# Kernel tuning notes

Measured on AMD Instinct MI355X. Metric: run time of the kernel, lower is better.

## Reference

```python
import jax, jax.numpy as jnp
import numpy as np

B, S, E, H, L = 16, 1024, 512, 8, 4
D = E // H  # head_dim = 64


def setup_inputs() -> dict:
    key = jax.random.key(0)
    ks = jax.random.split(key, 16)
    std = 0.02
    inp = {
        "q": jax.random.normal(ks[0], (B, S, E), jnp.float32),
        "k": jax.random.normal(ks[1], (B, S, E), jnp.float32),
        "v": jax.random.normal(ks[2], (B, S, E), jnp.float32),
        # standard Linear params (torch convention: W is (out, in))
        "Wq": jax.random.normal(ks[3], (E, E), jnp.float32) * std,
        "bq": jnp.zeros((E,), jnp.float32),
        "Wk": jax.random.normal(ks[4], (E, E), jnp.float32) * std,
        "bk": jnp.zeros((E,), jnp.float32),
        # WFLinear: shared weight elementwise-multiplied by per-language factor
        "Wv_share": jax.random.normal(ks[5], (E, E), jnp.float32) * std,
        "Wv_spec": 1.0 + jax.random.normal(ks[6], (L, E, E), jnp.float32) * std,
        "bv_share": jnp.zeros((E,), jnp.float32),
        "bv_spec": jax.random.normal(ks[7], (L, E), jnp.float32) * std,
        "Wo_share": jax.random.normal(ks[8], (E, E), jnp.float32) * std,
        "Wo_spec": 1.0 + jax.random.normal(ks[9], (L, E, E), jnp.float32) * std,
        "bo_share": jnp.zeros((E,), jnp.float32),
        "bo_spec": jax.random.normal(ks[10], (L, E), jnp.float32) * std,
        "mask": jax.random.randint(ks[11], (B, S), 0, 2, jnp.int32),
        "languageID": 1,
    }
    return inp


def reference(q, k, v, Wq, bq, Wk, bk, Wv_share, Wv_spec, bv_share, bv_spec,
              Wo_share, Wo_spec, bo_share, bo_spec, mask, languageID):
    scaling = D ** (-0.5)
    # projections (torch Linear: x @ W.T + b)
    Q = (q @ Wq.T + bq).reshape(B, S, H, D).transpose(0, 2, 1, 3) * scaling
    K = (k @ Wk.T + bk).reshape(B, S, H, D).transpose(0, 2, 1, 3)
    Wv = Wv_share * Wv_spec[languageID]
    bv = bv_share + bv_spec[languageID]
    V = (v @ Wv.T + bv).reshape(B, S, H, D).transpose(0, 2, 1, 3)
    # NOTE: faithful to original — Q already scaled by d_k^-0.5, and
    # AttentionWF divides by sqrt(d_k) AGAIN (effective scale 1/d_k).
    alpha = jnp.einsum("bhqd,bhkd->bhqk", Q, K) / np.float32(np.sqrt(D))
    m = (mask == 0)[:, None, None, :]  # (B,1,1,S) over key axis
    alpha = jnp.where(m, jnp.float32(-1e9), alpha)
    alpha = jax.nn.softmax(alpha, axis=-1)
    # dropout p=0.0 -> identity
    ctx = jnp.einsum("bhqk,bhkd->bhqd", alpha, V)  # (B,H,S,D)
    concat = ctx.transpose(0, 2, 1, 3).reshape(B, S, E)
    Wo = Wo_share * Wo_spec[languageID]
    bo = bo_share + bo_spec[languageID]
    return concat @ Wo.T + bo
```

## Files before the change

### kernel.cpp

```cpp
#include <hip/hip_runtime.h>

#define B_ 16
#define S_ 1024
#define E_ 512
#define H_ 8
#define D_ 64
#define L_ 4
#define M_ (B_*S_)

typedef unsigned short u16;
typedef __attribute__((ext_vector_type(8))) short bf16x8;
typedef __attribute__((ext_vector_type(4))) float f32x4;

__device__ __forceinline__ u16 f2bf(float x) {
  unsigned u = __float_as_uint(x);
  unsigned r = (u + 0x7fffu + ((u >> 16) & 1u)) >> 16;
  return (u16)r;
}
__device__ __forceinline__ ushort4 f2bf4(float4 f) {
  ushort4 u;
  u.x = f2bf(f.x); u.y = f2bf(f.y); u.z = f2bf(f.z); u.w = f2bf(f.w);
  return u;
}

typedef __attribute__((address_space(1))) const void gconst_void;
typedef __attribute__((address_space(3))) void lds_void;
__device__ __forceinline__ void gl_lds16(const u16* g, u16* l) {
  __builtin_amdgcn_global_load_lds((gconst_void*)g, (lds_void*)l, 16, 0, 0);
}

__global__ __launch_bounds__(256) void cvt3(
    const float* __restrict__ a, const float* __restrict__ b, const float* __restrict__ c,
    u16* __restrict__ da, u16* __restrict__ db, u16* __restrict__ dc) {
  int i = blockIdx.x * 256 + threadIdx.x;
  const float* s = (blockIdx.y == 0) ? a : (blockIdx.y == 1) ? b : c;
  u16* d = (blockIdx.y == 0) ? da : (blockIdx.y == 1) ? db : dc;
  ((ushort4*)d)[i] = f2bf4(((const float4*)s)[i]);
}

__global__ __launch_bounds__(256) void prep_w(
    const float* __restrict__ Wq, const float* __restrict__ Wk,
    const float* __restrict__ Wv_sh, const float* __restrict__ Wv_sp,
    const float* __restrict__ Wo_sh, const float* __restrict__ Wo_sp,
    const float* __restrict__ bv_sh, const float* __restrict__ bv_sp,
    const float* __restrict__ bo_sh, const float* __restrict__ bo_sp,
    const int* __restrict__ langp,
    u16* __restrict__ Wq_b, u16* __restrict__ Wk_b,
    u16* __restrict__ Wv_b, u16* __restrict__ Wo_b,
    float* __restrict__ bv_f, float* __restrict__ bo_f) {
  int lang = langp[0];
  int i = blockIdx.x * 256 + threadIdx.x;
  size_t wofs = (size_t)lang * (E_*E_/4) + i;
  ((ushort4*)Wq_b)[i] = f2bf4(((const float4*)Wq)[i]);
  ((ushort4*)Wk_b)[i] = f2bf4(((const float4*)Wk)[i]);
  float4 vs = ((const float4*)Wv_sh)[i], vp = ((const float4*)Wv_sp)[wofs];
  float4 os = ((const float4*)Wo_sh)[i], op = ((const float4*)Wo_sp)[wofs];
  float4 vv = {vs.x*vp.x, vs.y*vp.y, vs.z*vp.z, vs.w*vp.w};
  float4 oo = {os.x*op.x, os.y*op.y, os.z*op.z, os.w*op.w};
  ((ushort4*)Wv_b)[i] = f2bf4(vv);
  ((ushort4*)Wo_b)[i] = f2bf4(oo);
  if (i < E_/4) {
    float4 b1 = ((const float4*)bv_sh)[i], b2 = ((const float4*)(bv_sp + (size_t)lang*E_))[i];
    float4 b3 = ((const float4*)bo_sh)[i], b4 = ((const float4*)(bo_sp + (size_t)lang*E_))[i];
    float4 r1 = {b1.x+b2.x, b1.y+b2.y, b1.z+b2.z, b1.w+b2.w};
    float4 r2 = {b3.x+b4.x, b3.y+b4.y, b3.z+b4.z, b3.w+b4.w};
    ((float4*)bv_f)[i] = r1;
    ((float4*)bo_f)[i] = r2;
  }
}

__global__ __launch_bounds__(256) void gemm_lds(
    const u16* __restrict__ A, const u16* __restrict__ Bw,
    const float* __restrict__ bias,
    void* __restrict__ out, int out_bf16, int Mdim, int Ndim, int Kdim) {
  __shared__ u16 sA[128*32];
  __shared__ u16 sB[128*32];
  const int t = threadIdx.x;
  const int m0 = blockIdx.y * 128, n0 = blockIdx.x * 128;
  const int lane = t & 63, wid = t >> 6;
  const int m16 = lane & 15, qq = lane >> 4;
  const int wrow = (wid >> 1) * 64, wcol = (wid & 1) * 64;
  f32x4 acc[4][4] = {};
  const int c0 = 2*wid, c1 = 2*wid + 1;
  const int colk = (lane & 3) * 8;
  const int r0 = c0*16 + (lane >> 2), r1 = c1*16 + (lane >> 2);
  const u16* a0 = A  + (size_t)(m0 + r0) * Kdim + colk;
  const u16* a1 = A  + (size_t)(m0 + r1) * Kdim + colk;
  const u16* b0 = Bw + (size_t)(n0 + r0) * Kdim + colk;
  const u16* b1 = Bw + (size_t)(n0 + r1) * Kdim + colk;
  u16* sa0 = &sA[c0*512]; u16* sa1 = &sA[c1*512];
  u16* sb0 = &sB[c0*512]; u16* sb1 = &sB[c1*512];
  for (int k0 = 0; k0 < Kdim; k0 += 32) {
    gl_lds16(a0, sa0);
    gl_lds16(a1, sa1);
    gl_lds16(b0, sb0);
    gl_lds16(b1, sb1);
    __syncthreads();
    bf16x8 af[4], bfm[4];
#pragma unroll
    for (int mt = 0; mt < 4; ++mt)
      af[mt] = *(const bf16x8*)&sA[(wrow + mt*16 + m16) * 32 + qq*8];
#pragma unroll
    for (int nt = 0; nt < 4; ++nt)
      bfm[nt] = *(const bf16x8*)&sB[(wcol + nt*16 + m16) * 32 + qq*8];
#pragma unroll
    for (int mt = 0; mt < 4; ++mt)
#pragma unroll
      for (int nt = 0; nt < 4; ++nt)
        acc[mt][nt] = __builtin_amdgcn_mfma_f32_16x16x32_bf16(af[mt], bfm[nt], acc[mt][nt], 0, 0, 0);
    __syncthreads();
    a0 += 32; a1 += 32; b0 += 32; b1 += 32;
  }
  float bv[4];
#pragma unroll
  for (int nt = 0; nt < 4; ++nt) bv[nt] = bias[n0 + wcol + nt*16 + m16];
#pragma unroll
  for (int mt = 0; mt < 4; ++mt) {
    int gm = m0 + wrow + mt*16 + qq*4;
#pragma unroll
    for (int nt = 0; nt < 4; ++nt) {
      int gn = n0 + wcol + nt*16 + m16;
#pragma unroll
      for (int r = 0; r < 4; ++r) {
        float v = acc[mt][nt][r] + bv[nt];
        if (out_bf16) ((u16*)out)[(size_t)(gm + r) * Ndim + gn] = f2bf(v);
        else          ((float*)out)[(size_t)(gm + r) * Ndim + gn] = v;
      }
    }
  }
}

#define TS_ 72
__global__ __launch_bounds__(256) void transpose_v(const u16* __restrict__ Vb,
                                                   u16* __restrict__ Vt) {
  __shared__ u16 sT[64*TS_];
  const int t = threadIdx.x;
  const int bh = blockIdx.y, b = bh >> 3, h = bh & 7;
  const int s0 = blockIdx.x * 64;
  const int row = t >> 2, c0 = (t & 3) * 16;
  const u16* src = Vb + (size_t)(b*S_ + s0 + row) * E_ + h*D_ + c0;
  *(uint4*)&sT[row*TS_ + c0]     = *(const uint4*)src;
  *(uint4*)&sT[row*TS_ + c0 + 8] = *(const uint4*)(src + 8);
  __syncthreads();
  const int d = t >> 2, sc = (t & 3) * 16;
  unsigned w[8];
#pragma unroll
  for (int i = 0; i < 8; ++i) {
    unsigned lo = sT[(sc + 2*i    ) * TS_ + d];
    unsigned hi = sT[(sc + 2*i + 1) * TS_ + d];
    w[i] = lo | (hi << 16);
  }
  u16* dst = Vt + ((size_t)(b*H_ + h) * D_ + d) * S_ + s0 + sc;
  uint4 p0 = {w[0], w[1], w[2], w[3]}, p1 = {w[4], w[5], w[6], w[7]};
  *(uint4*)dst = p0;
  *(uint4*)(dst + 8) = p1;
}

#define KST 72
__global__ __launch_bounds__(256) void attn_mfma(
    const u16* __restrict__ Qb, const u16* __restrict__ Kb, const u16* __restrict__ Vt,
    const int* __restrict__ mask, u16* __restrict__ ctxb) {
  __shared__ u16 sK[64*KST];
  __shared__ u16 sV[64*KST];
  __shared__ u16 sP[64*KST];
  __shared__ float sMask[64];
  const int t = threadIdx.x;
  const int lane = t & 63, w = t >> 6;
  const int m16 = lane & 15, quad = lane >> 4;
  const int bh = blockIdx.y, b = bh >> 3, h = bh & 7;
  const int qblk = blockIdx.x * 64;
  const int q0 = qblk + w * 16;
  bf16x8 qf0, qf1;
  {
    const u16* qp = Qb + (size_t)(b*S_ + q0 + m16) * E_ + h*D_ + quad*8;
    qf0 = *(const bf16x8*)qp;
    qf1 = *(const bf16x8*)(qp + 32);
  }
  f32x4 oacc[4] = {};
  float lpart[4] = {0.f, 0.f, 0.f, 0.f};
  const int srow = t >> 2, sc0 = (t & 3) * 16;
  const u16* kp = Kb + (size_t)(b*S_ + srow) * E_ + h*D_ + sc0;
  const u16* vp = Vt + ((size_t)(b*H_ + h) * D_ + srow) * S_ + sc0;
  uint4 rk0 = *(const uint4*)kp, rk1 = *(const uint4*)(kp + 8);
  uint4 rv0 = *(const uint4*)vp, rv1 = *(const uint4*)(vp + 8);
  float rmsk = 0.f;
  if (t < 64) rmsk = (mask[b*S_ + t] == 0) ? -1e9f : 0.f;
  const float CS = 0.015625f * 1.44269504f;
  for (int kt = 0; kt < S_; kt += 64) {
    *(uint4*)&sK[srow*KST + sc0]     = rk0;
    *(uint4*)&sK[srow*KST + sc0 + 8] = rk1;
    *(uint4*)&sV[srow*KST + sc0]     = rv0;
    *(uint4*)&sV[srow*KST + sc0 + 8] = rv1;
    if (t < 64) sMask[t] = rmsk;
    __syncthreads();
    if (kt + 64 < S_) {
      kp += (size_t)64 * E_; vp += 64;
      rk0 = *(const uint4*)kp; rk1 = *(const uint4*)(kp + 8);
      rv0 = *(const uint4*)vp; rv1 = *(const uint4*)(vp + 8);
      if (t < 64) rmsk = (mask[b*S_ + kt + 64 + t] == 0) ? -1e9f : 0.f;
    }
    f32x4 sacc[4] = {};
#pragma unroll
    for (int ct = 0; ct < 4; ++ct) {
      bf16x8 kf0 = *(const bf16x8*)&sK[(ct*16 + m16)*KST + quad*8];
      bf16x8 kf1 = *(const bf16x8*)&sK[(ct*16 + m16)*KST + 32 + quad*8];
      sacc[ct] = __builtin_amdgcn_mfma_f32_16x16x32_bf16(qf0, kf0, sacc[ct], 0, 0, 0);
      sacc[ct] = __builtin_amdgcn_mfma_f32_16x16x32_bf16(qf1, kf1, sacc[ct], 0, 0, 0);
    }
    float madd[4];
#pragma unroll
    for (int ct = 0; ct < 4; ++ct) madd[ct] = sMask[ct*16 + m16];
#pragma unroll
    for (int r = 0; r < 4; ++r) {
      float p0 = exp2f(fmaf(sacc[0][r], CS, madd[0]));
      float p1 = exp2f(fmaf(sacc[1][r], CS, madd[1]));
      float p2 = exp2f(fmaf(sacc[2][r], CS, madd[2]));
      float p3 = exp2f(fmaf(sacc[3][r], CS, madd[3]));
      lpart[r] += (p0 + p1) + (p2 + p3);
      sP[(w*16 + quad*4 + r)*KST +       m16] = f2bf(p0);
      sP[(w*16 + quad*4 + r)*KST + 16 + m16] = f2bf(p1);
      sP[(w*16 + quad*4 + r)*KST + 32 + m16] = f2bf(p2);
      sP[(w*16 + quad*4 + r)*KST + 48 + m16] = f2bf(p3);
    }
    bf16x8 pf0 = *(const bf16x8*)&sP[(w*16 + m16)*KST + quad*8];
    bf16x8 pf1 = *(const bf16x8*)&sP[(w*16 + m16)*KST + 32 + quad*8];
#pragma unroll
    for (int dt = 0; dt < 4; ++dt) {
      bf16x8 vf0 = *(const bf16x8*)&sV[(dt*16 + m16)*KST + quad*8];
      bf16x8 vf1 = *(const bf16x8*)&sV[(dt*16 + m16)*KST + 32 + quad*8];
      oacc[dt] = __builtin_amdgcn_mfma_f32_16x16x32_bf16(pf0, vf0, oacc[dt], 0, 0, 0);
      oacc[dt] = __builtin_amdgcn_mfma_f32_16x16x32_bf16(pf1, vf1, oacc[dt], 0, 0, 0);
    }
    __syncthreads();
  }
  float inv[4];
#pragma unroll
  for (int r = 0; r < 4; ++r) {
    float l = lpart[r];
    l += __shfl_xor(l, 1);
    l += __shfl_xor(l, 2);
    l += __shfl_xor(l, 4);
    l += __shfl_xor(l, 8);
    inv[r] = 1.0f / l;
  }
#pragma unroll
  for (int dt = 0; dt < 4; ++dt)
#pragma unroll
    for (int r = 0; r < 4; ++r)
      sP[(w*16 + quad*4 + r)*KST + dt*16 + m16] = f2bf(oacc[dt][r] * inv[r]);
  __syncthreads();
  const int orow = t >> 2, oc0 = (t & 3) * 16;
  uint4 o0 = *(uint4*)&sP[orow*KST + oc0];
  uint4 o1 = *(uint4*)&sP[orow*KST + oc0 + 8];
  u16* dst = ctxb + (size_t)(b*S_ + qblk + orow) * E_ + h*D_ + oc0;
  *(uint4*)dst = o0;
  *(uint4*)(dst + 8) = o1;
}

extern "C" void kernel_launch(void* const* d_in, const int* in_sizes, int n_in,
                              void* d_out, int out_size, void* d_ws, size_t ws_size,
                              hipStream_t stream) {
  const float* q     = (const float*)d_in[0];
  const float* k     = (const float*)d_in[1];
  const float* v     = (const float*)d_in[2];
  const float* Wq    = (const float*)d_in[3];
  const float* bq    = (const float*)d_in[4];
  const float* Wk    = (const float*)d_in[5];
  const float* bk    = (const float*)d_in[6];
  const float* Wv_sh = (const float*)d_in[7];
  const float* Wv_sp = (const float*)d_in[8];
  const float* bv_sh = (const float*)d_in[9];
  const float* bv_sp = (const float*)d_in[10];
  const float* Wo_sh = (const float*)d_in[11];
  const float* Wo_sp = (const float*)d_in[12];
  const float* bo_sh = (const float*)d_in[13];
  const float* bo_sp = (const float*)d_in[14];
  const int*   mask  = (const int*)d_in[15];
  const int*   lang  = (const int*)d_in[16];

  char* ws = (char*)d_ws;
  size_t off = 0;
  auto alloc = [&](size_t bytes) -> char* {
    char* p = ws + off;
    off += (bytes + 255) & ~(size_t)255;
    return p;
  };
  u16* qb   = (u16*)alloc((size_t)M_ * E_ * 2);
  u16* kb   = (u16*)alloc((size_t)M_ * E_ * 2);
  u16* vb   = (u16*)alloc((size_t)M_ * E_ * 2);
  u16* Qb   = (u16*)alloc((size_t)M_ * E_ * 2);
  u16* Kb   = (u16*)alloc((size_t)M_ * E_ * 2);
  u16* Vb   = (u16*)alloc((size_t)M_ * E_ * 2);
  u16* Vt   = (u16*)alloc((size_t)M_ * E_ * 2);
  u16* ctxb = (u16*)alloc((size_t)M_ * E_ * 2);
  u16* Wq_b = (u16*)alloc((size_t)E_ * E_ * 2);
  u16* Wk_b = (u16*)alloc((size_t)E_ * E_ * 2);
  u16* Wv_b = (u16*)alloc((size_t)E_ * E_ * 2);
  u16* Wo_b = (u16*)alloc((size_t)E_ * E_ * 2);
  float* bv_f = (float*)alloc(E_ * 4);
  float* bo_f = (float*)alloc(E_ * 4);

  prep_w<<<E_*E_/1024, 256, 0, stream>>>(Wq, Wk, Wv_sh, Wv_sp, Wo_sh, Wo_sp,
                                         bv_sh, bv_sp, bo_sh, bo_sp, lang,
                                         Wq_b, Wk_b, Wv_b, Wo_b, bv_f, bo_f);
  cvt3<<<dim3(M_*E_/1024, 3), 256, 0, stream>>>(q, k, v, qb, kb, vb);

  dim3 ggrid(E_/128, M_/128);
  gemm_lds<<<ggrid, 256, 0, stream>>>(qb, Wq_b, bq,   Qb, 1, M_, E_, E_);
  gemm_lds<<<ggrid, 256, 0, stream>>>(kb, Wk_b, bk,   Kb, 1, M_, E_, E_);
  gemm_lds<<<ggrid, 256, 0, stream>>>(vb, Wv_b, bv_f, Vb, 1, M_, E_, E_);

  dim3 tgrid(S_/64, B_*H_);
  transpose_v<<<tgrid, 256, 0, stream>>>(Vb, Vt);

  dim3 agrid(S_/64, B_*H_);
  attn_mfma<<<agrid, 256, 0, stream>>>(Qb, Kb, Vt, mask, ctxb);

  gemm_lds<<<ggrid, 256, 0, stream>>>(ctxb, Wo_b, bo_f, d_out, 0, M_, E_, E_);
}
```

Measured before the change: 337.2 us.

## Fuse fp32-to-bf16 input conversion into batched QKV GEMM and transpose S tile

Removes the separate cvt3 conversion kernel and its bf16 input buffers. A new gemm_qkv kernel loads fp32 activations straight into LDS and converts them to bf16 while building MFMA fragments, and it handles all three projections in one launch through blockIdx.z. The attention kernel swaps the MFMA operand order so each lane holds 4 consecutive keys, writes P with packed 64-bit stores, and reduces the row sum through LDS. The trade-off is twice the LDS and global traffic per A tile from fp32 loads, plus truncating-style rounding in pk_bf16 (it adds 0x8000 with no tie-to-even handling).

```diff
diff --git a/kernel.cpp b/kernel.cpp
--- a/kernel.cpp
+++ b/kernel.cpp
@@ -11,6 +11,7 @@
 typedef unsigned short u16;
 typedef __attribute__((ext_vector_type(8))) short bf16x8;
 typedef __attribute__((ext_vector_type(4))) float f32x4;
+typedef __attribute__((ext_vector_type(4))) unsigned uint4v;
 
 __device__ __forceinline__ u16 f2bf(float x) {
   unsigned u = __float_as_uint(x);
@@ -22,20 +23,20 @@
   u.x = f2bf(f.x); u.y = f2bf(f.y); u.z = f2bf(f.z); u.w = f2bf(f.w);
   return u;
 }
+__device__ __forceinline__ unsigned pk_bf16(float lo, float hi) {
+  unsigned ul = __float_as_uint(lo) + 0x8000u;
+  unsigned uh = __float_as_uint(hi) + 0x8000u;
+#if __has_builtin(__builtin_amdgcn_perm)
+  return __builtin_amdgcn_perm(uh, ul, 0x07060302u);
+#else
+  return (ul >> 16) | (uh & 0xffff0000u);
+#endif
+}
 
 typedef __attribute__((address_space(1))) const void gconst_void;
 typedef __attribute__((address_space(3))) void lds_void;
-__device__ __forceinline__ void gl_lds16(const u16* g, u16* l) {
+__device__ __forceinline__ void gl_lds16(const void* g, void* l) {
   __builtin_amdgcn_global_load_lds((gconst_void*)g, (lds_void*)l, 16, 0, 0);
-}
-
-__global__ __launch_bounds__(256) void cvt3(
-    const float* __restrict__ a, const float* __restrict__ b, const float* __restrict__ c,
-    u16* __restrict__ da, u16* __restrict__ db, u16* __restrict__ dc) {
-  int i = blockIdx.x * 256 + threadIdx.x;
-  const float* s = (blockIdx.y == 0) ? a : (blockIdx.y == 1) ? b : c;
-  u16* d = (blockIdx.y == 0) ? da : (blockIdx.y == 1) ? db : dc;
-  ((ushort4*)d)[i] = f2bf4(((const float4*)s)[i]);
 }
 
 __global__ __launch_bounds__(256) void prep_w(
@@ -69,12 +70,89 @@
   }
 }
 
+__global__ __launch_bounds__(256) void gemm_qkv(
+    const float* __restrict__ q, const float* __restrict__ k, const float* __restrict__ v,
+    const u16* __restrict__ Wq_b, const u16* __restrict__ Wk_b, const u16* __restrict__ Wv_b,
+    const float* __restrict__ bq, const float* __restrict__ bk, const float* __restrict__ bv,
+    u16* __restrict__ Qb, u16* __restrict__ Kb, u16* __restrict__ Vb) {
+  __shared__ __align__(16) float sAf[128*32];
+  __shared__ __align__(16) u16 sB[128*32];
+  const int z = blockIdx.z;
+  const float* A    = (z == 0) ? q : (z == 1) ? k : v;
+  const u16*   Bw   = (z == 0) ? Wq_b : (z == 1) ? Wk_b : Wv_b;
+  const float* bias = (z == 0) ? bq : (z == 1) ? bk : bv;
+  u16*         out  = (z == 0) ? Qb : (z == 1) ? Kb : Vb;
+  const int t = threadIdx.x;
+  const int m0 = blockIdx.y * 128, n0 = blockIdx.x * 128;
+  const int lane = t & 63, wid = t >> 6;
+  const int m16 = lane & 15, qq = lane >> 4;
+  const int wrow = (wid >> 1) * 64, wcol = (wid & 1) * 64;
+  f32x4 acc[4][4] = {};
+  const int ca0 = wid*4;
+  const float* ap[4];
+  float* sap[4];
+#pragma unroll
+  for (int i = 0; i < 4; ++i) {
+    int ca = ca0 + i;
+    ap[i]  = A + (size_t)(m0 + ca*8 + (lane >> 3)) * E_ + (lane & 7) * 4;
+    sap[i] = &sAf[ca * 256];
+  }
+  const int cb0 = wid*2, cb1 = wid*2 + 1;
+  const u16* bp0 = Bw + (size_t)(n0 + cb0*16 + (lane >> 2)) * E_ + (lane & 3) * 8;
+  const u16* bp1 = Bw + (size_t)(n0 + cb1*16 + (lane >> 2)) * E_ + (lane & 3) * 8;
+  u16* sbp0 = &sB[cb0 * 512];
+  u16* sbp1 = &sB[cb1 * 512];
+  for (int k0 = 0; k0 < E_; k0 += 32) {
+#pragma unroll
+    for (int i = 0; i < 4; ++i) gl_lds16(ap[i], sap[i]);
+    gl_lds16(bp0, sbp0);
+    gl_lds16(bp1, sbp1);
+    __syncthreads();
+    bf16x8 af[4], bfm[4];
+#pragma unroll
+    for (int mt = 0; mt < 4; ++mt) {
+      const float* ar = &sAf[(wrow + mt*16 + m16) * 32 + qq*8];
+      f32x4 a0 = *(const f32x4*)ar;
+      f32x4 a1 = *(const f32x4*)(ar + 4);
+      union { uint4v u; bf16x8 h; } cv;
+      cv.u = (uint4v){ pk_bf16(a0[0], a0[1]), pk_bf16(a0[2], a0[3]),
+                       pk_bf16(a1[0], a1[1]), pk_bf16(a1[2], a1[3]) };
+      af[mt] = cv.h;
+    }
+#pragma unroll
+    for (int nt = 0; nt < 4; ++nt)
+      bfm[nt] = *(const bf16x8*)&sB[(wcol + nt*16 + m16) * 32 + qq*8];
+#pragma unroll
+    for (int mt = 0; mt < 4; ++mt)
+#pragma unroll
+      for (int nt = 0; nt < 4; ++nt)
+        acc[mt][nt] = __builtin_amdgcn_mfma_f32_16x16x32_bf16(af[mt], bfm[nt], acc[mt][nt], 0, 0, 0);
+    __syncthreads();
+#pragma unroll
+    for (int i = 0; i < 4; ++i) ap[i] += 32;
+    bp0 += 32; bp1 += 32;
+  }
+  float bvv[4];
+#pragma unroll
+  for (int nt = 0; nt < 4; ++nt) bvv[nt] = bias[n0 + wcol + nt*16 + m16];
+#pragma unroll
+  for (int mt = 0; mt < 4; ++mt) {
+    int gm = m0 + wrow + mt*16 + qq*4;
+#pragma unroll
+    for (int nt = 0; nt < 4; ++nt) {
+      int gn = n0 + wcol + nt*16 + m16;
+#pragma unroll
+      for (int r = 0; r < 4; ++r)
+        out[(size_t)(gm + r) * E_ + gn] = f2bf(acc[mt][nt][r] + bvv[nt]);
+    }
+  }
+}
+
 __global__ __launch_bounds__(256) void gemm_lds(
     const u16* __restrict__ A, const u16* __restrict__ Bw,
-    const float* __restrict__ bias,
-    void* __restrict__ out, int out_bf16, int Mdim, int Ndim, int Kdim) {
-  __shared__ u16 sA[128*32];
-  __shared__ u16 sB[128*32];
+    const float* __restrict__ bias, float* __restrict__ out) {
+  __shared__ __align__(16) u16 sA[128*32];
+  __shared__ __align__(16) u16 sB[128*32];
   const int t = threadIdx.x;
   const int m0 = blockIdx.y * 128, n0 = blockIdx.x * 128;
   const int lane = t & 63, wid = t >> 6;
@@ -84,13 +162,13 @@
   const int c0 = 2*wid, c1 = 2*wid + 1;
   const int colk = (lane & 3) * 8;
   const int r0 = c0*16 + (lane >> 2), r1 = c1*16 + (lane >> 2);
-  const u16* a0 = A  + (size_t)(m0 + r0) * Kdim + colk;
-  const u16* a1 = A  + (size_t)(m0 + r1) * Kdim + colk;
-  const u16* b0 = Bw + (size_t)(n0 + r0) * Kdim + colk;
-  const u16* b1 = Bw + (size_t)(n0 + r1) * Kdim + colk;
+  const u16* a0 = A  + (size_t)(m0 + r0) * E_ + colk;
+  const u16* a1 = A  + (size_t)(m0 + r1) * E_ + colk;
+  const u16* b0 = Bw + (size_t)(n0 + r0) * E_ + colk;
+  const u16* b1 = Bw + (size_t)(n0 + r1) * E_ + colk;
   u16* sa0 = &sA[c0*512]; u16* sa1 = &sA[c1*512];
   u16* sb0 = &sB[c0*512]; u16* sb1 = &sB[c1*512];
-  for (int k0 = 0; k0 < Kdim; k0 += 32) {
+  for (int k0 = 0; k0 < E_; k0 += 32) {
     gl_lds16(a0, sa0);
     gl_lds16(a1, sa1);
     gl_lds16(b0, sb0);
@@ -121,11 +199,8 @@
     for (int nt = 0; nt < 4; ++nt) {
       int gn = n0 + wcol + nt*16 + m16;
 #pragma unroll
-      for (int r = 0; r < 4; ++r) {
-        float v = acc[mt][nt][r] + bv[nt];
-        if (out_bf16) ((u16*)out)[(size_t)(gm + r) * Ndim + gn] = f2bf(v);
-        else          ((float*)out)[(size_t)(gm + r) * Ndim + gn] = v;
-      }
+      for (int r = 0; r < 4; ++r)
+        out[(size_t)(gm + r) * E_ + gn] = acc[mt][nt][r] + bv[nt];
     }
   }
 }
@@ -133,7 +208,7 @@
 #define TS_ 72
 __global__ __launch_bounds__(256) void transpose_v(const u16* __restrict__ Vb,
                                                    u16* __restrict__ Vt) {
-  __shared__ u16 sT[64*TS_];
+  __shared__ __align__(16) u16 sT[64*TS_];
   const int t = threadIdx.x;
   const int bh = blockIdx.y, b = bh >> 3, h = bh & 7;
   const int s0 = blockIdx.x * 64;
@@ -160,10 +235,11 @@
 __global__ __launch_bounds__(256) void attn_mfma(
     const u16* __restrict__ Qb, const u16* __restrict__ Kb, const u16* __restrict__ Vt,
     const int* __restrict__ mask, u16* __restrict__ ctxb) {
-  __shared__ u16 sK[64*KST];
-  __shared__ u16 sV[64*KST];
-  __shared__ u16 sP[64*KST];
-  __shared__ float sMask[64];
+  __shared__ __align__(16) u16 sK[64*KST];
+  __shared__ __align__(16) u16 sV[64*KST];
+  __shared__ __align__(16) u16 sP[64*KST];
+  __shared__ __align__(16) float sMask[64];
+  __shared__ __align__(16) float sL[64];
   const int t = threadIdx.x;
   const int lane = t & 63, w = t >> 6;
   const int m16 = lane & 15, quad = lane >> 4;
@@ -177,7 +253,7 @@
     qf1 = *(const bf16x8*)(qp + 32);
   }
   f32x4 oacc[4] = {};
-  float lpart[4] = {0.f, 0.f, 0.f, 0.f};
+  float lpart = 0.f;
   const int srow = t >> 2, sc0 = (t & 3) * 16;
   const u16* kp = Kb + (size_t)(b*S_ + srow) * E_ + h*D_ + sc0;
   const u16* vp = Vt + ((size_t)(b*H_ + h) * D_ + srow) * S_ + sc0;
@@ -204,23 +280,19 @@
     for (int ct = 0; ct < 4; ++ct) {
       bf16x8 kf0 = *(const bf16x8*)&sK[(ct*16 + m16)*KST + quad*8];
       bf16x8 kf1 = *(const bf16x8*)&sK[(ct*16 + m16)*KST + 32 + quad*8];
-      sacc[ct] = __builtin_amdgcn_mfma_f32_16x16x32_bf16(qf0, kf0, sacc[ct], 0, 0, 0);
-      sacc[ct] = __builtin_amdgcn_mfma_f32_16x16x32_bf16(qf1, kf1, sacc[ct], 0, 0, 0);
-    }
-    float madd[4];
-#pragma unroll
-    for (int ct = 0; ct < 4; ++ct) madd[ct] = sMask[ct*16 + m16];
-#pragma unroll
-    for (int r = 0; r < 4; ++r) {
-      float p0 = exp2f(fmaf(sacc[0][r], CS, madd[0]));
-      float p1 = exp2f(fmaf(sacc[1][r], CS, madd[1]));
-      float p2 = exp2f(fmaf(sacc[2][r], CS, madd[2]));
-      float p3 = exp2f(fmaf(sacc[3][r], CS, madd[3]));
-      lpart[r] += (p0 + p1) + (p2 + p3);
-      sP[(w*16 + quad*4 + r)*KST +       m16] = f2bf(p0);
-      sP[(w*16 + quad*4 + r)*KST + 16 + m16] = f2bf(p1);
-      sP[(w*16 + quad*4 + r)*KST + 32 + m16] = f2bf(p2);
-      sP[(w*16 + quad*4 + r)*KST + 48 + m16] = f2bf(p3);
+      sacc[ct] = __builtin_amdgcn_mfma_f32_16x16x32_bf16(kf0, qf0, sacc[ct], 0, 0, 0);
+      sacc[ct] = __builtin_amdgcn_mfma_f32_16x16x32_bf16(kf1, qf1, sacc[ct], 0, 0, 0);
+    }
+#pragma unroll
+    for (int ct = 0; ct < 4; ++ct) {
+      f32x4 msk = *(const f32x4*)&sMask[ct*16 + quad*4];
+      float p0 = exp2f(fmaf(sacc[ct][0], CS, msk[0]));
+      float p1 = exp2f(fmaf(sacc[ct][1], CS, msk[1]));
+      float p2 = exp2f(fmaf(sacc[ct][2], CS, msk[2]));
+      float p3 = exp2f(fmaf(sacc[ct][3], CS, msk[3]));
+      lpart += (p0 + p1) + (p2 + p3);
+      uint2 pq = { pk_bf16(p0, p1), pk_bf16(p2, p3) };
+      *(uint2*)&sP[(w*16 + m16)*KST + ct*16 + quad*4] = pq;
     }
     bf16x8 pf0 = *(const bf16x8*)&sP[(w*16 + m16)*KST + quad*8];
     bf16x8 pf1 = *(const bf16x8*)&sP[(w*16 + m16)*KST + 32 + quad*8];
@@ -233,16 +305,12 @@
     }
     __syncthreads();
   }
+  lpart += __shfl_xor(lpart, 16);
+  lpart += __shfl_xor(lpart, 32);
+  if (quad == 0) sL[w*16 + m16] = lpart;
   float inv[4];
 #pragma unroll
-  for (int r = 0; r < 4; ++r) {
-    float l = lpart[r];
-    l += __shfl_xor(l, 1);
-    l += __shfl_xor(l, 2);
-    l += __shfl_xor(l, 4);
-    l += __shfl_xor(l, 8);
-    inv[r] = 1.0f / l;
-  }
+  for (int r = 0; r < 4; ++r) inv[r] = 1.0f / sL[w*16 + quad*4 + r];
 #pragma unroll
   for (int dt = 0; dt < 4; ++dt)
 #pragma unroll
@@ -285,9 +353,6 @@
     off += (bytes + 255) & ~(size_t)255;
     return p;
   };
-  u16* qb   = (u16*)alloc((size_t)M_ * E_ * 2);
-  u16* kb   = (u16*)alloc((size_t)M_ * E_ * 2);
-  u16* vb   = (u16*)alloc((size_t)M_ * E_ * 2);
   u16* Qb   = (u16*)alloc((size_t)M_ * E_ * 2);
   u16* Kb   = (u16*)alloc((size_t)M_ * E_ * 2);
   u16* Vb   = (u16*)alloc((size_t)M_ * E_ * 2);
@@ -303,12 +368,10 @@
   prep_w<<<E_*E_/1024, 256, 0, stream>>>(Wq, Wk, Wv_sh, Wv_sp, Wo_sh, Wo_sp,
                                          bv_sh, bv_sp, bo_sh, bo_sp, lang,
                                          Wq_b, Wk_b, Wv_b, Wo_b, bv_f, bo_f);
-  cvt3<<<dim3(M_*E_/1024, 3), 256, 0, stream>>>(q, k, v, qb, kb, vb);
-
-  dim3 ggrid(E_/128, M_/128);
-  gemm_lds<<<ggrid, 256, 0, stream>>>(qb, Wq_b, bq,   Qb, 1, M_, E_, E_);
-  gemm_lds<<<ggrid, 256, 0, stream>>>(kb, Wk_b, bk,   Kb, 1, M_, E_, E_);
-  gemm_lds<<<ggrid, 256, 0, stream>>>(vb, Wv_b, bv_f, Vb, 1, M_, E_, E_);
+
+  dim3 qkvgrid(E_/128, M_/128, 3);
+  gemm_qkv<<<qkvgrid, 256, 0, stream>>>(q, k, v, Wq_b, Wk_b, Wv_b,
+                                        bq, bk, bv_f, Qb, Kb, Vb);
 
   dim3 tgrid(S_/64, B_*H_);
   transpose_v<<<tgrid, 256, 0, stream>>>(Vb, Vt);
@@ -316,5 +379,6 @@
   dim3 agrid(S_/64, B_*H_);
   attn_mfma<<<agrid, 256, 0, stream>>>(Qb, Kb, Vt, mask, ctxb);
 
-  gemm_lds<<<ggrid, 256, 0, stream>>>(ctxb, Wo_b, bo_f, d_out, 0, M_, E_, E_);
-}
+  dim3 ggrid(E_/128, M_/128);
+  gemm_lds<<<ggrid, 256, 0, stream>>>(ctxb, Wo_b, bo_f, (float*)d_out);
+}
```

After: 316.9 us. 1.06x faster.
